# Kernel tuning notes

Measured on AMD Instinct MI355X. Metric: run time of the kernel, lower is better.

Reference implementation:

```python
import jax, jax.numpy as jnp
import numpy as np

N_TX = 1_000_000   # transaction nodes
N_W  = 250_000     # wallet nodes
E    = 2_000_000   # edges per relation
F_TX, F_W = 64, 32 # raw feature dims
H, OUT = 64, 2     # hidden, out (module defaults)


def setup_inputs() -> dict:
    key = jax.random.key(0)
    ks = jax.random.split(key, 40)
    f32 = jnp.float32
    def w(i, shape):
        return jax.random.normal(ks[i], shape, dtype=f32) * 0.05
    inp = {}
    inp["x_tx"] = jax.random.normal(ks[0], (N_TX, F_TX), dtype=f32)
    inp["x_w"]  = jax.random.normal(ks[1], (N_W, F_W), dtype=f32)
    inp["src_tw"] = jax.random.randint(ks[2], (E,), 0, N_TX)
    inp["dst_tw"] = jax.random.randint(ks[3], (E,), 0, N_W)
    inp["src_wt"] = jax.random.randint(ks[4], (E,), 0, N_W)
    inp["dst_wt"] = jax.random.randint(ks[5], (E,), 0, N_TX)
    # lin_in per node type
    inp["Win_tx"], inp["bin_tx"] = w(6, (F_TX, H)), w(7, (H,))
    inp["Win_w"],  inp["bin_w"]  = w(8, (F_W, H)),  w(9, (H,))
    # conv1: SAGEConv per edge type (lin_l has bias, lin_r no bias)
    inp["Wl1_tw"], inp["bl1_tw"], inp["Wr1_tw"] = w(10, (H, H)), w(11, (H,)), w(12, (H, H))
    inp["Wl1_wt"], inp["bl1_wt"], inp["Wr1_wt"] = w(13, (H, H)), w(14, (H,)), w(15, (H, H))
    # conv2
    inp["Wl2_tw"], inp["bl2_tw"], inp["Wr2_tw"] = w(16, (H, H)), w(17, (H,)), w(18, (H, H))
    inp["Wl2_wt"], inp["bl2_wt"], inp["Wr2_wt"] = w(19, (H, H)), w(20, (H,)), w(21, (H, H))
    # tx head
    inp["Wh1"], inp["bh1"] = w(22, (H, H)), w(23, (H,))
    inp["Wh2"], inp["bh2"] = w(24, (H, OUT)), w(25, (OUT,))
    return inp


def _sage(x_src, x_dst, src, dst, Wl, bl, Wr, n_dst):
    # PyG SAGEConv: lin_l(mean_{j->i} x_src[j]) + lin_r(x_dst[i])
    agg = jax.ops.segment_sum(x_src[src], dst, num_segments=n_dst)
    cnt = jax.ops.segment_sum(jnp.ones((src.shape[0],), x_src.dtype), dst,
                              num_segments=n_dst)
    mean = agg / jnp.maximum(cnt, 1.0)[:, None]
    return mean @ Wl + bl + x_dst @ Wr


def reference(x_tx, x_w, src_tw, dst_tw, src_wt, dst_wt,
              Win_tx, bin_tx, Win_w, bin_w,
              Wl1_tw, bl1_tw, Wr1_tw, Wl1_wt, bl1_wt, Wr1_wt,
              Wl2_tw, bl2_tw, Wr2_tw, Wl2_wt, bl2_wt, Wr2_wt,
              Wh1, bh1, Wh2, bh2):
    # per-type input projection
    h_tx = x_tx @ Win_tx + bin_tx   # [N_TX, H]
    h_w  = x_w @ Win_w + bin_w      # [N_W, H]
    # conv1 (HeteroConv aggr='sum'; each dst type has one relation) + relu
    w1 = jax.nn.relu(_sage(h_tx, h_w,  src_tw, dst_tw, Wl1_tw, bl1_tw, Wr1_tw, N_W))
    t1 = jax.nn.relu(_sage(h_w,  h_tx, src_wt, dst_wt, Wl1_wt, bl1_wt, Wr1_wt, N_TX))
    # conv2 + relu
    w2 = jax.nn.relu(_sage(t1, w1, src_tw, dst_tw, Wl2_tw, bl2_tw, Wr2_tw, N_W))
    t2 = jax.nn.relu(_sage(w1, t1, src_wt, dst_wt, Wl2_wt, bl2_wt, Wr2_wt, N_TX))
    # tx head (dropout inactive in eval)
    logits = jax.nn.relu(t2 @ Wh1 + bh1) @ Wh2 + bh2  # [N_TX, 2]
    return (logits, t2, w2)
```

## Files before the change

### kernel.cpp

```cpp
#include <hip/hip_runtime.h>
#include <hip/hip_bf16.h>

typedef __hip_bfloat16 bf16;
typedef __attribute__((ext_vector_type(8))) short bf16x8;
typedef __attribute__((ext_vector_type(4))) float f32x4;

__device__ __forceinline__ float b2f(bf16 v) { return __bfloat162float(v); }
__device__ __forceinline__ bf16 f2b(float v) { return __float2bfloat16(v); }
__device__ __forceinline__ unsigned short f2bb(float v) {
    unsigned int u = __float_as_uint(v);
    u += 0x7fffu + ((u >> 16) & 1u);
    return (unsigned short)(u >> 16);
}
__device__ __forceinline__ float b2fx(bf16x8 v, int k) {
    return __uint_as_float(((unsigned int)(unsigned short)v[k]) << 16);
}

__device__ __forceinline__ f32x4 mfma16(bf16x8 a, bf16x8 b, f32x4 c) {
    return __builtin_amdgcn_mfma_f32_16x16x32_bf16(a, b, c, 0, 0, 0);
}

__device__ __forceinline__ bf16x8 load_bfrag(const float* __restrict__ W, int k0, int col) {
    bf16x8 f;
#pragma unroll
    for (int j = 0; j < 8; ++j)
        f[j] = (short)f2bb(W[(size_t)(k0 + j) * 64 + col]);
    return f;
}

__device__ __forceinline__ int swzH(int row, int b) {
    return row * 128 + (b ^ ((row & 7) << 4));
}

__global__ void count2_kernel(const int* __restrict__ dst_tw, int* __restrict__ deg_w, int ne_tw,
                              const int* __restrict__ dst_wt, int* __restrict__ deg_tx, int ne_wt) {
    int e = blockIdx.x * 256 + threadIdx.x;
    if (e < ne_tw) atomicAdd(&deg_w[dst_tw[e]], 1);
    else {
        int e2 = e - ne_tw;
        if (e2 < ne_wt) atomicAdd(&deg_tx[dst_wt[e2]], 1);
    }
}

__global__ void scan1m_kernel(const int* __restrict__ dw, int* __restrict__ ew,
                              int* __restrict__ pw, int nw, int npw,
                              const int* __restrict__ dt, int* __restrict__ et,
                              int* __restrict__ pt, int nt) {
    __shared__ int sT[256];
    const int* deg; int* excl; int* partial; int n; int b;
    if ((int)blockIdx.x < npw) { deg = dw; excl = ew; partial = pw; n = nw; b = blockIdx.x; }
    else { deg = dt; excl = et; partial = pt; n = nt; b = blockIdx.x - npw; }
    int tid = threadIdx.x;
    int base = b * 1024 + tid * 4;
    int v0 = (base + 0 < n) ? deg[base + 0] : 0;
    int v1 = (base + 1 < n) ? deg[base + 1] : 0;
    int v2 = (base + 2 < n) ? deg[base + 2] : 0;
    int v3 = (base + 3 < n) ? deg[base + 3] : 0;
    int t = v0 + v1 + v2 + v3;
    sT[tid] = t;
    __syncthreads();
    for (int off = 1; off < 256; off <<= 1) {
        int x = (tid >= off) ? sT[tid - off] : 0;
        __syncthreads();
        sT[tid] += x;
        __syncthreads();
    }
    int et2 = sT[tid] - t;
    if (tid == 255) partial[b] = sT[255];
    if (base + 0 < n) excl[base + 0] = et2;
    if (base + 1 < n) excl[base + 1] = et2 + v0;
    if (base + 2 < n) excl[base + 2] = et2 + v0 + v1;
    if (base + 3 < n) excl[base + 3] = et2 + v0 + v1 + v2;
}

__global__ void scan2m_kernel(int* __restrict__ pw, int npw, int* __restrict__ pt, int npt) {
    __shared__ int sT[256];
    __shared__ int carry;
    int* partial = blockIdx.x ? pt : pw;
    int np = blockIdx.x ? npt : npw;
    int tid = threadIdx.x;
    if (tid == 0) carry = 0;
    __syncthreads();
    for (int c = 0; c < np; c += 256) {
        int i = c + tid;
        int v = (i < np) ? partial[i] : 0;
        sT[tid] = v;
        __syncthreads();
        for (int off = 1; off < 256; off <<= 1) {
            int x = (tid >= off) ? sT[tid - off] : 0;
            __syncthreads();
            sT[tid] += x;
            __syncthreads();
        }
        int incl = sT[tid];
        int total = sT[255];
        if (i < np) partial[i] = carry + incl - v;
        __syncthreads();
        if (tid == 0) carry += total;
        __syncthreads();
    }
}

__global__ void scan3m_kernel(const int* __restrict__ ew, const int* __restrict__ pw,
                              int* __restrict__ rw, int* __restrict__ cw, int nw, int nbw,
                              const int* __restrict__ et, const int* __restrict__ pt,
                              int* __restrict__ rt, int* __restrict__ ct, int nt) {
    int b = blockIdx.x;
    const int* excl; const int* partial; int* rp; int* cur; int n; int i;
    if (b < nbw) { i = b * 256 + threadIdx.x; excl = ew; partial = pw; rp = rw; cur = cw; n = nw; }
    else { i = (b - nbw) * 256 + threadIdx.x; excl = et; partial = pt; rp = rt; cur = ct; n = nt; }
    if (i < n) {
        int v = excl[i] + partial[i >> 10];
        rp[i] = v;
        cur[i] = v;
    }
}

__global__ void scatter2_kernel(const int* __restrict__ src_tw, const int* __restrict__ dst_tw,
                                int* __restrict__ cur_w, int* __restrict__ col_tw, int ne_tw,
                                const int* __restrict__ src_wt, const int* __restrict__ dst_wt,
                                int* __restrict__ cur_tx, int* __restrict__ col_wt, int ne_wt) {
    int e = blockIdx.x * 256 + threadIdx.x;
    if (e < ne_tw) {
        int p = atomicAdd(&cur_w[dst_tw[e]], 1);
        col_tw[p] = src_tw[e];
    } else {
        int e2 = e - ne_tw;
        if (e2 < ne_wt) {
            int p = atomicAdd(&cur_tx[dst_wt[e2]], 1);
            col_wt[p] = src_wt[e2];
        }
    }
}

#define GM_ACC(x, w) \
    a0 += (w) * b2fx(x, 0); a1 += (w) * b2fx(x, 1); \
    a2 += (w) * b2fx(x, 2); a3 += (w) * b2fx(x, 3); \
    a4 += (w) * b2fx(x, 4); a5 += (w) * b2fx(x, 5); \
    a6 += (w) * b2fx(x, 6); a7 += (w) * b2fx(x, 7);

__device__ __forceinline__ void gather_body(const bf16* __restrict__ h,
                                            const int* __restrict__ rowptr,
                                            const int* __restrict__ deg,
                                            const int* __restrict__ col,
                                            bf16* __restrict__ mean, int n, int bid) {
    int tid = threadIdx.x;
    int row = bid * 32 + (tid >> 3);
    if (row >= n) return;
    int fg = tid & 7;
    int base = rowptr[row];
    int d = deg[row];
    int lasto = (d > 0) ? d - 1 : 0;
    float a0 = 0.f, a1 = 0.f, a2 = 0.f, a3 = 0.f;
    float a4 = 0.f, a5 = 0.f, a6 = 0.f, a7 = 0.f;
    for (int e0 = 0; e0 < d; e0 += 8) {
        int o1 = (e0 + 1 < d) ? e0 + 1 : lasto;
        int o2 = (e0 + 2 < d) ? e0 + 2 : lasto;
        int o3 = (e0 + 3 < d) ? e0 + 3 : lasto;
        int o4 = (e0 + 4 < d) ? e0 + 4 : lasto;
        int o5 = (e0 + 5 < d) ? e0 + 5 : lasto;
        int o6 = (e0 + 6 < d) ? e0 + 6 : lasto;
        int o7 = (e0 + 7 < d) ? e0 + 7 : lasto;
        int s0 = col[base + e0], s1 = col[base + o1];
        int s2 = col[base + o2], s3 = col[base + o3];
        int s4 = col[base + o4], s5 = col[base + o5];
        int s6 = col[base + o6], s7 = col[base + o7];
        bf16x8 x0 = *(const bf16x8*)(h + ((size_t)s0 << 6) + (fg << 3));
        bf16x8 x1 = *(const bf16x8*)(h + ((size_t)s1 << 6) + (fg << 3));
        bf16x8 x2 = *(const bf16x8*)(h + ((size_t)s2 << 6) + (fg << 3));
        bf16x8 x3 = *(const bf16x8*)(h + ((size_t)s3 << 6) + (fg << 3));
        bf16x8 x4 = *(const bf16x8*)(h + ((size_t)s4 << 6) + (fg << 3));
        bf16x8 x5 = *(const bf16x8*)(h + ((size_t)s5 << 6) + (fg << 3));
        bf16x8 x6 = *(const bf16x8*)(h + ((size_t)s6 << 6) + (fg << 3));
        bf16x8 x7 = *(const bf16x8*)(h + ((size_t)s7 << 6) + (fg << 3));
        float w1 = (e0 + 1 < d) ? 1.f : 0.f;
        float w2 = (e0 + 2 < d) ? 1.f : 0.f;
        float w3 = (e0 + 3 < d) ? 1.f : 0.f;
        float w4 = (e0 + 4 < d) ? 1.f : 0.f;
        float w5 = (e0 + 5 < d) ? 1.f : 0.f;
        float w6 = (e0 + 6 < d) ? 1.f : 0.f;
        float w7 = (e0 + 7 < d) ? 1.f : 0.f;
        GM_ACC(x0, 1.f)
        GM_ACC(x1, w1)
        GM_ACC(x2, w2)
        GM_ACC(x3, w3)
        GM_ACC(x4, w4)
        GM_ACC(x5, w5)
        GM_ACC(x6, w6)
        GM_ACC(x7, w7)
    }
    float dd = fmaxf((float)d, 1.f);
    bf16x8 o;
    o[0] = (short)f2bb(a0 / dd); o[1] = (short)f2bb(a1 / dd);
    o[2] = (short)f2bb(a2 / dd); o[3] = (short)f2bb(a3 / dd);
    o[4] = (short)f2bb(a4 / dd); o[5] = (short)f2bb(a5 / dd);
    o[6] = (short)f2bb(a6 / dd); o[7] = (short)f2bb(a7 / dd);
    *(bf16x8*)(mean + ((size_t)row << 6) + (fg << 3)) = o;
}

__global__ __launch_bounds__(256)
void gather2_kernel(const bf16* __restrict__ hw, const int* __restrict__ rpw,
                    const int* __restrict__ dw, const int* __restrict__ cw,
                    bf16* __restrict__ mw, int nw, int gbw,
                    const bf16* __restrict__ ht, const int* __restrict__ rpt,
                    const int* __restrict__ dt, const int* __restrict__ ct,
                    bf16* __restrict__ mt, int nt) {
    if ((int)blockIdx.x < gbw) gather_body(hw, rpw, dw, cw, mw, nw, blockIdx.x);
    else                       gather_body(ht, rpt, dt, ct, mt, nt, blockIdx.x - gbw);
}

template<bool HEAD>
__device__ __forceinline__ void sage_body(
        const bf16* __restrict__ mean, const bf16* __restrict__ xd,
        const float* __restrict__ Wl, const float* __restrict__ bl,
        const float* __restrict__ Wr,
        float* __restrict__ outf, bf16* __restrict__ outb,
        const float* __restrict__ Wh1, const float* __restrict__ bh1,
        const float* __restrict__ Wh2, const float* __restrict__ bh2,
        float* __restrict__ logits, int n, int bid, short* sH) {
    int tid = threadIdx.x;
    int lane = tid & 63, w = tid >> 6;
    int lm = lane & 15, lq = lane >> 4;

    bf16x8 wc[4][4];
    bf16x8 wh[4][2];
    float blv[4], h1v[4], w2a[4], w2b[4];
#pragma unroll
    for (int ct = 0; ct < 4; ++ct) {
        int colc = ct * 16 + lm;
        wc[ct][0] = load_bfrag(Wl, lq * 8, colc);
        wc[ct][1] = load_bfrag(Wl, 32 + lq * 8, colc);
        wc[ct][2] = load_bfrag(Wr, lq * 8, colc);
        wc[ct][3] = load_bfrag(Wr, 32 + lq * 8, colc);
        blv[ct] = bl[colc];
        if (HEAD) {
            wh[ct][0] = load_bfrag(Wh1, lq * 8, colc);
            wh[ct][1] = load_bfrag(Wh1, 32 + lq * 8, colc);
            h1v[ct] = bh1[colc];
            w2a[ct] = Wh2[colc * 2 + 0];
            w2b[ct] = Wh2[colc * 2 + 1];
        }
    }
    float b20 = 0.f, b21 = 0.f;
    if (HEAD) { b20 = bh2[0]; b21 = bh2[1]; }

    int larow = w * 16 + lm;
    int row0 = bid * 512;
    if (row0 >= n) return;
    int ar = row0 + larow; ar = (ar < n) ? ar : (n - 1);
    const bf16* mrow = mean + ((size_t)ar << 6);
    const bf16* xrow = xd + ((size_t)ar << 6);
    bf16x8 a0 = *(const bf16x8*)(mrow + lq * 8);
    bf16x8 a1 = *(const bf16x8*)(mrow + 32 + lq * 8);
    bf16x8 a2 = *(const bf16x8*)(xrow + lq * 8);
    bf16x8 a3 = *(const bf16x8*)(xrow + 32 + lq * 8);

    for (int g = 0; g < 8; ++g) {
        int gr0 = row0 + g * 64;
        if (gr0 >= n) break;
        bf16x8 n0 = a0, n1 = a1, n2 = a2, n3 = a3;
        if (g < 7) {
            int nr = gr0 + 64 + larow; nr = (nr < n) ? nr : (n - 1);
            const bf16* nm = mean + ((size_t)nr << 6);
            const bf16* nx = xd + ((size_t)nr << 6);
            n0 = *(const bf16x8*)(nm + lq * 8);
            n1 = *(const bf16x8*)(nm + 32 + lq * 8);
            n2 = *(const bf16x8*)(nx + lq * 8);
            n3 = *(const bf16x8*)(nx + 32 + lq * 8);
        }
#pragma unroll
        for (int ct = 0; ct < 4; ++ct) {
            f32x4 acc = {0.f, 0.f, 0.f, 0.f};
            acc = mfma16(a0, wc[ct][0], acc);
            acc = mfma16(a1, wc[ct][1], acc);
            acc = mfma16(a2, wc[ct][2], acc);
            acc = mfma16(a3, wc[ct][3], acc);
            int colc = ct * 16 + lm;
#pragma unroll
            for (int r = 0; r < 4; ++r) {
                int lrow = w * 16 + lq * 4 + r;
                int grow = gr0 + lrow;
                float v = fmaxf(acc[r] + blv[ct], 0.f);
                if (grow < n) {
                    if (outf) outf[(size_t)grow * 64 + colc] = v;
                    if (outb) outb[(size_t)grow * 64 + colc] = f2b(v);
                }
                if (HEAD)
                    *(short*)((char*)sH + swzH(lrow, colc * 2)) = (short)f2bb(v);
            }
        }
        if (HEAD) {
            bf16x8 h0 = *(const bf16x8*)((char*)sH + swzH(larow, lq * 16));
            bf16x8 h1 = *(const bf16x8*)((char*)sH + swzH(larow, 64 + lq * 16));
            float qa0 = 0.f, qa1 = 0.f, qa2 = 0.f, qa3 = 0.f;
            float qb0 = 0.f, qb1 = 0.f, qb2 = 0.f, qb3 = 0.f;
#pragma unroll
            for (int ct = 0; ct < 4; ++ct) {
                f32x4 acc = {0.f, 0.f, 0.f, 0.f};
                acc = mfma16(h0, wh[ct][0], acc);
                acc = mfma16(h1, wh[ct][1], acc);
                float hb = h1v[ct];
                float h_0 = fmaxf(acc[0] + hb, 0.f);
                float h_1 = fmaxf(acc[1] + hb, 0.f);
                float h_2 = fmaxf(acc[2] + hb, 0.f);
                float h_3 = fmaxf(acc[3] + hb, 0.f);
                qa0 += h_0 * w2a[ct]; qb0 += h_0 * w2b[ct];
                qa1 += h_1 * w2a[ct]; qb1 += h_1 * w2b[ct];
                qa2 += h_2 * w2a[ct]; qb2 += h_2 * w2b[ct];
                qa3 += h_3 * w2a[ct]; qb3 += h_3 * w2b[ct];
            }
#pragma unroll
            for (int m = 8; m; m >>= 1) {
                qa0 += __shfl_xor(qa0, m); qb0 += __shfl_xor(qb0, m);
                qa1 += __shfl_xor(qa1, m); qb1 += __shfl_xor(qb1, m);
                qa2 += __shfl_xor(qa2, m); qb2 += __shfl_xor(qb2, m);
                qa3 += __shfl_xor(qa3, m); qb3 += __shfl_xor(qb3, m);
            }
            int rowb = gr0 + w * 16 + lq * 4;
            if (lm == 0) {
                if (rowb + 0 < n) { logits[(size_t)(rowb + 0) * 2 + 0] = qa0 + b20;
                                    logits[(size_t)(rowb + 0) * 2 + 1] = qb0 + b21; }
                if (rowb + 1 < n) { logits[(size_t)(rowb + 1) * 2 + 0] = qa1 + b20;
                                    logits[(size_t)(rowb + 1) * 2 + 1] = qb1 + b21; }
                if (rowb + 2 < n) { logits[(size_t)(rowb + 2) * 2 + 0] = qa2 + b20;
                                    logits[(size_t)(rowb + 2) * 2 + 1] = qb2 + b21; }
                if (rowb + 3 < n) { logits[(size_t)(rowb + 3) * 2 + 0] = qa3 + b20;
                                    logits[(size_t)(rowb + 3) * 2 + 1] = qb3 + b21; }
            }
        }
        a0 = n0; a1 = n1; a2 = n2; a3 = n3;
    }
}

template<bool HEAD>
__global__ __launch_bounds__(256, 2)
void sage2_kernel(const bf16* __restrict__ mw, const bf16* __restrict__ xw,
                  const float* __restrict__ Wlw, const float* __restrict__ blw,
                  const float* __restrict__ Wrw,
                  float* __restrict__ outfw, bf16* __restrict__ outbw, int nw, int gbw,
                  const bf16* __restrict__ mt, const bf16* __restrict__ xt,
                  const float* __restrict__ Wlt, const float* __restrict__ blt,
                  const float* __restrict__ Wrt,
                  float* __restrict__ outft, bf16* __restrict__ outbt,
                  const float* __restrict__ Wh1, const float* __restrict__ bh1,
                  const float* __restrict__ Wh2, const float* __restrict__ bh2,
                  float* __restrict__ logits, int nt) {
    __shared__ __align__(16) short sH[HEAD ? 64 * 64 : 8];
    if ((int)blockIdx.x < gbw)
        sage_body<false>(mw, xw, Wlw, blw, Wrw, outfw, outbw,
                         nullptr, nullptr, nullptr, nullptr, nullptr, nw, blockIdx.x, sH);
    else
        sage_body<HEAD>(mt, xt, Wlt, blt, Wrt, outft, outbt,
                        Wh1, bh1, Wh2, bh2, logits, nt, blockIdx.x - gbw, sH);
}

__global__ __launch_bounds__(256)
void proj64_mfma_kernel(const float* __restrict__ x, const float* __restrict__ W,
                        const float* __restrict__ b, bf16* __restrict__ out, int n) {
    int tid = threadIdx.x;
    int lane = tid & 63, w = tid >> 6;
    int lm = lane & 15, lq = lane >> 4;

    bf16x8 wc[4][2];
    float bv[4];
#pragma unroll
    for (int ct = 0; ct < 4; ++ct) {
        int colc = ct * 16 + lm;
        wc[ct][0] = load_bfrag(W, lq * 8, colc);
        wc[ct][1] = load_bfrag(W, 32 + lq * 8, colc);
        bv[ct] = b[colc];
    }

    int larow = w * 16 + lm;
    int row0 = blockIdx.x * 512;
    if (row0 >= n) return;
    int ar = row0 + larow; ar = (ar < n) ? ar : (n - 1);
    const float* xrow = x + ((size_t)ar << 6);
    float4 p0 = *(const float4*)(xrow + lq * 8);
    float4 p1 = *(const float4*)(xrow + lq * 8 + 4);
    float4 p2 = *(const float4*)(xrow + 32 + lq * 8);
    float4 p3 = *(const float4*)(xrow + 32 + lq * 8 + 4);

    for (int g = 0; g < 8; ++g) {
        int gr0 = row0 + g * 64;
        if (gr0 >= n) break;
        float4 q0 = p0, q1 = p1, q2 = p2, q3 = p3;
        if (g < 7) {
            int nr = gr0 + 64 + larow; nr = (nr < n) ? nr : (n - 1);
            const float* nx = x + ((size_t)nr << 6);
            q0 = *(const float4*)(nx + lq * 8);
            q1 = *(const float4*)(nx + lq * 8 + 4);
            q2 = *(const float4*)(nx + 32 + lq * 8);
            q3 = *(const float4*)(nx + 32 + lq * 8 + 4);
        }
        bf16x8 a0, a1;
        a0[0] = (short)f2bb(p0.x); a0[1] = (short)f2bb(p0.y);
        a0[2] = (short)f2bb(p0.z); a0[3] = (short)f2bb(p0.w);
        a0[4] = (short)f2bb(p1.x); a0[5] = (short)f2bb(p1.y);
        a0[6] = (short)f2bb(p1.z); a0[7] = (short)f2bb(p1.w);
        a1[0] = (short)f2bb(p2.x); a1[1] = (short)f2bb(p2.y);
        a1[2] = (short)f2bb(p2.z); a1[3] = (short)f2bb(p2.w);
        a1[4] = (short)f2bb(p3.x); a1[5] = (short)f2bb(p3.y);
        a1[6] = (short)f2bb(p3.z); a1[7] = (short)f2bb(p3.w);
#pragma unroll
        for (int ct = 0; ct < 4; ++ct) {
            f32x4 acc = {0.f, 0.f, 0.f, 0.f};
            acc = mfma16(a0, wc[ct][0], acc);
            acc = mfma16(a1, wc[ct][1], acc);
            int colc = ct * 16 + lm;
#pragma unroll
            for (int r = 0; r < 4; ++r) {
                int grow = gr0 + w * 16 + lq * 4 + r;
                if (grow < n)
                    out[(size_t)grow * 64 + colc] = f2b(acc[r] + bv[ct]);
            }
        }
        p0 = q0; p1 = q1; p2 = q2; p3 = q3;
    }
}

template<int F>
__global__ void proj_kernel(const float* __restrict__ x, const float* __restrict__ W,
                            const float* __restrict__ b, bf16* __restrict__ out, int n) {
    __shared__ float sW[F][64];
    __shared__ float sb[64];
    __shared__ float sx[16][F];
    int tid = threadIdx.x;
    for (int idx = tid; idx < F * 16; idx += 256)
        ((float4*)sW)[idx] = ((const float4*)W)[idx];
    if (tid < 64) sb[tid] = b[tid];
    int base = blockIdx.x * 64;
    int w = tid >> 6, j = tid & 63;
    int lw = w * 4;
    for (int g = 0; g < 4; ++g) {
        int row0 = base + g * 16;
        __syncthreads();
        for (int idx = tid; idx < 4 * F; idx += 256) {
            int rr = idx / (F / 4), c4 = idx - rr * (F / 4);
            int row = row0 + rr;
            float4 v = (row < n) ? ((const float4*)x)[(size_t)row * (F / 4) + c4]
                                 : make_float4(0.f, 0.f, 0.f, 0.f);
            *(float4*)&sx[rr][c4 * 4] = v;
        }
        __syncthreads();
        float a0 = sb[j], a1 = sb[j], a2 = sb[j], a3 = sb[j];
#pragma unroll 2
        for (int k = 0; k < F; k += 4) {
            float w0 = sW[k][j], w1 = sW[k + 1][j], w2 = sW[k + 2][j], w3 = sW[k + 3][j];
            float4 m0 = *(const float4*)&sx[lw + 0][k];
            float4 m1 = *(const float4*)&sx[lw + 1][k];
            float4 m2 = *(const float4*)&sx[lw + 2][k];
            float4 m3 = *(const float4*)&sx[lw + 3][k];
            a0 += m0.x * w0 + m0.y * w1 + m0.z * w2 + m0.w * w3;
            a1 += m1.x * w0 + m1.y * w1 + m1.z * w2 + m1.w * w3;
            a2 += m2.x * w0 + m2.y * w1 + m2.z * w2 + m2.w * w3;
            a3 += m3.x * w0 + m3.y * w1 + m3.z * w2 + m3.w * w3;
        }
        int r0 = row0 + lw;
        if (r0 + 0 < n) out[(size_t)(r0 + 0) * 64 + j] = f2b(a0);
        if (r0 + 1 < n) out[(size_t)(r0 + 1) * 64 + j] = f2b(a1);
        if (r0 + 2 < n) out[(size_t)(r0 + 2) * 64 + j] = f2b(a2);
        if (r0 + 3 < n) out[(size_t)(r0 + 3) * 64 + j] = f2b(a3);
    }
}

extern "C" void kernel_launch(void* const* d_in, const int* in_sizes, int n_in,
                              void* d_out, int out_size, void* d_ws, size_t ws_size,
                              hipStream_t stream) {
    const float* x_tx   = (const float*)d_in[0];
    const float* x_w    = (const float*)d_in[1];
    const int*   src_tw = (const int*)d_in[2];
    const int*   dst_tw = (const int*)d_in[3];
    const int*   src_wt = (const int*)d_in[4];
    const int*   dst_wt = (const int*)d_in[5];
    const float* Win_tx = (const float*)d_in[6];
    const float* bin_tx = (const float*)d_in[7];
    const float* Win_w  = (const float*)d_in[8];
    const float* bin_w  = (const float*)d_in[9];
    const float* Wl1_tw = (const float*)d_in[10];
    const float* bl1_tw = (const float*)d_in[11];
    const float* Wr1_tw = (const float*)d_in[12];
    const float* Wl1_wt = (const float*)d_in[13];
    const float* bl1_wt = (const float*)d_in[14];
    const float* Wr1_wt = (const float*)d_in[15];
    const float* Wl2_tw = (const float*)d_in[16];
    const float* bl2_tw = (const float*)d_in[17];
    const float* Wr2_tw = (const float*)d_in[18];
    const float* Wl2_wt = (const float*)d_in[19];
    const float* bl2_wt = (const float*)d_in[20];
    const float* Wr2_wt = (const float*)d_in[21];
    const float* Wh1    = (const float*)d_in[22];
    const float* bh1    = (const float*)d_in[23];
    const float* Wh2    = (const float*)d_in[24];
    const float* bh2    = (const float*)d_in[25];

    const int n_tx  = in_sizes[0] / 64;
    const int n_w   = in_sizes[1] / 32;
    const int ne_tw = in_sizes[2];
    const int ne_wt = in_sizes[4];

    bf16* mean_tx = (bf16*)d_ws;
    bf16* mean_w  = mean_tx + (size_t)n_tx * 64;
    bf16* A       = mean_w + (size_t)n_w * 64;
    bf16* B       = A + (size_t)n_tx * 64;
    int*  deg_w   = (int*)(B + (size_t)n_w * 64);
    int*  deg_tx  = deg_w + n_w;
    int*  rp_w    = deg_tx + n_tx;
    int*  rp_tx   = rp_w + n_w;
    int*  cur_w   = rp_tx + n_tx;
    int*  cur_tx  = cur_w + n_w;
    int*  col_tw  = cur_tx + n_tx;
    int*  col_wt  = col_tw + ne_tw;
    int*  part_w  = col_wt + ne_wt;
    int*  part_tx = part_w + 4096;

    float* out_logits = (float*)d_out;
    float* out_t2 = out_logits + (size_t)n_tx * 2;
    float* out_w2 = out_t2 + (size_t)n_tx * 64;

    dim3 blk(256);
    int grid_proj_tx = (n_tx + 511) / 512;
    int grid_proj_w  = (n_w + 63) / 64;
    int gs_w  = (n_w + 511) / 512;
    int gs_tx = (n_tx + 511) / 512;
    int gg_w  = (n_w + 31) / 32;
    int gg_tx = (n_tx + 31) / 32;
    int grid_e = (ne_tw + ne_wt + 255) / 256;
    int np_w  = (n_w + 1023) / 1024;
    int np_tx = (n_tx + 1023) / 1024;
    int nbw = (n_w + 255) / 256;
    int nbt = (n_tx + 255) / 256;

    hipMemsetAsync(deg_w, 0, (size_t)n_w * sizeof(int), stream);
    hipMemsetAsync(deg_tx, 0, (size_t)n_tx * sizeof(int), stream);
    count2_kernel<<<grid_e, blk, 0, stream>>>(dst_tw, deg_w, ne_tw, dst_wt, deg_tx, ne_wt);
    scan1m_kernel<<<np_w + np_tx, blk, 0, stream>>>(deg_w, cur_w, part_w, n_w, np_w,
                                                    deg_tx, cur_tx, part_tx, n_tx);
    scan2m_kernel<<<2, blk, 0, stream>>>(part_w, np_w, part_tx, np_tx);
    scan3m_kernel<<<nbw + nbt, blk, 0, stream>>>(cur_w, part_w, rp_w, cur_w, n_w, nbw,
                                                 cur_tx, part_tx, rp_tx, cur_tx, n_tx);
    scatter2_kernel<<<grid_e, blk, 0, stream>>>(src_tw, dst_tw, cur_w, col_tw, ne_tw,
                                                src_wt, dst_wt, cur_tx, col_wt, ne_wt);

    proj64_mfma_kernel<<<grid_proj_tx, blk, 0, stream>>>(x_tx, Win_tx, bin_tx, A, n_tx);
    proj_kernel<32><<<grid_proj_w, blk, 0, stream>>>(x_w, Win_w, bin_w, B, n_w);

    gather2_kernel<<<gg_w + gg_tx, blk, 0, stream>>>(
        A, rp_w, deg_w, col_tw, mean_w, n_w, gg_w,
        B, rp_tx, deg_tx, col_wt, mean_tx, n_tx);
    sage2_kernel<false><<<gs_w + gs_tx, blk, 0, stream>>>(
        mean_w, B, Wl1_tw, bl1_tw, Wr1_tw, nullptr, B, n_w, gs_w,
        mean_tx, A, Wl1_wt, bl1_wt, Wr1_wt, nullptr, A,
        nullptr, nullptr, nullptr, nullptr, nullptr, n_tx);

    gather2_kernel<<<gg_w + gg_tx, blk, 0, stream>>>(
        A, rp_w, deg_w, col_tw, mean_w, n_w, gg_w,
        B, rp_tx, deg_tx, col_wt, mean_tx, n_tx);
    sage2_kernel<true><<<gs_w + gs_tx, blk, 0, stream>>>(
        mean_w, B, Wl2_tw, bl2_tw, Wr2_tw, out_w2, nullptr, n_w, gs_w,
        mean_tx, A, Wl2_wt, bl2_wt, Wr2_wt, out_t2, nullptr,
        Wh1, bh1, Wh2, bh2, out_logits, n_tx);
}
```

Measured before the change: 1.607 ms.

## Record edge ranks during count and fuse CSR scatter with input projections

The degree-count kernel now stores each edge's atomicAdd return value as its rank within its destination. The scatter step then writes col[rowptr[dst]+rank] with no second round of atomics, and the separate cursor array is dropped. The scatter and both input projection kernels are merged into one launch with block-range dispatch, so projection work can overlap the memory-bound scatter and two launches go away. The cost is extra rank arrays in workspace plus their write and read traffic, and the fused kernel always reserves the projection's shared memory, which can lower occupancy for the scatter blocks.

```diff
diff --git a/kernel.cpp b/kernel.cpp
--- a/kernel.cpp
+++ b/kernel.cpp
@@ -32,13 +32,15 @@
     return row * 128 + (b ^ ((row & 7) << 4));
 }
 
-__global__ void count2_kernel(const int* __restrict__ dst_tw, int* __restrict__ deg_w, int ne_tw,
-                              const int* __restrict__ dst_wt, int* __restrict__ deg_tx, int ne_wt) {
+__global__ void count_rank2_kernel(const int* __restrict__ dst_tw, int* __restrict__ deg_w,
+                                   int* __restrict__ rank_tw, int ne_tw,
+                                   const int* __restrict__ dst_wt, int* __restrict__ deg_tx,
+                                   int* __restrict__ rank_wt, int ne_wt) {
     int e = blockIdx.x * 256 + threadIdx.x;
-    if (e < ne_tw) atomicAdd(&deg_w[dst_tw[e]], 1);
+    if (e < ne_tw) rank_tw[e] = atomicAdd(&deg_w[dst_tw[e]], 1);
     else {
         int e2 = e - ne_tw;
-        if (e2 < ne_wt) atomicAdd(&deg_tx[dst_wt[e2]], 1);
+        if (e2 < ne_wt) rank_wt[e2] = atomicAdd(&deg_tx[dst_wt[e2]], 1);
     }
 }
 
@@ -102,34 +104,155 @@
 }
 
 __global__ void scan3m_kernel(const int* __restrict__ ew, const int* __restrict__ pw,
-                              int* __restrict__ rw, int* __restrict__ cw, int nw, int nbw,
+                              int* __restrict__ rw, int nw, int nbw,
                               const int* __restrict__ et, const int* __restrict__ pt,
-                              int* __restrict__ rt, int* __restrict__ ct, int nt) {
+                              int* __restrict__ rt, int nt) {
     int b = blockIdx.x;
-    const int* excl; const int* partial; int* rp; int* cur; int n; int i;
-    if (b < nbw) { i = b * 256 + threadIdx.x; excl = ew; partial = pw; rp = rw; cur = cw; n = nw; }
-    else { i = (b - nbw) * 256 + threadIdx.x; excl = et; partial = pt; rp = rt; cur = ct; n = nt; }
-    if (i < n) {
-        int v = excl[i] + partial[i >> 10];
-        rp[i] = v;
-        cur[i] = v;
-    }
-}
-
-__global__ void scatter2_kernel(const int* __restrict__ src_tw, const int* __restrict__ dst_tw,
-                                int* __restrict__ cur_w, int* __restrict__ col_tw, int ne_tw,
-                                const int* __restrict__ src_wt, const int* __restrict__ dst_wt,
-                                int* __restrict__ cur_tx, int* __restrict__ col_wt, int ne_wt) {
-    int e = blockIdx.x * 256 + threadIdx.x;
-    if (e < ne_tw) {
-        int p = atomicAdd(&cur_w[dst_tw[e]], 1);
-        col_tw[p] = src_tw[e];
+    const int* excl; const int* partial; int* rp; int n; int i;
+    if (b < nbw) { i = b * 256 + threadIdx.x; excl = ew; partial = pw; rp = rw; n = nw; }
+    else { i = (b - nbw) * 256 + threadIdx.x; excl = et; partial = pt; rp = rt; n = nt; }
+    if (i < n) rp[i] = excl[i] + partial[i >> 10];
+}
+
+__device__ __forceinline__ void proj64_body(const float* __restrict__ x,
+                                            const float* __restrict__ W,
+                                            const float* __restrict__ b,
+                                            bf16* __restrict__ out, int n, int bid) {
+    int tid = threadIdx.x;
+    int lane = tid & 63, w = tid >> 6;
+    int lm = lane & 15, lq = lane >> 4;
+
+    bf16x8 wc[4][2];
+    float bv[4];
+#pragma unroll
+    for (int ct = 0; ct < 4; ++ct) {
+        int colc = ct * 16 + lm;
+        wc[ct][0] = load_bfrag(W, lq * 8, colc);
+        wc[ct][1] = load_bfrag(W, 32 + lq * 8, colc);
+        bv[ct] = b[colc];
+    }
+
+    int larow = w * 16 + lm;
+    int row0 = bid * 512;
+    if (row0 >= n) return;
+    int ar = row0 + larow; ar = (ar < n) ? ar : (n - 1);
+    const float* xrow = x + ((size_t)ar << 6);
+    float4 p0 = *(const float4*)(xrow + lq * 8);
+    float4 p1 = *(const float4*)(xrow + lq * 8 + 4);
+    float4 p2 = *(const float4*)(xrow + 32 + lq * 8);
+    float4 p3 = *(const float4*)(xrow + 32 + lq * 8 + 4);
+
+    for (int g = 0; g < 8; ++g) {
+        int gr0 = row0 + g * 64;
+        if (gr0 >= n) break;
+        float4 q0 = p0, q1 = p1, q2 = p2, q3 = p3;
+        if (g < 7) {
+            int nr = gr0 + 64 + larow; nr = (nr < n) ? nr : (n - 1);
+            const float* nx = x + ((size_t)nr << 6);
+            q0 = *(const float4*)(nx + lq * 8);
+            q1 = *(const float4*)(nx + lq * 8 + 4);
+            q2 = *(const float4*)(nx + 32 + lq * 8);
+            q3 = *(const float4*)(nx + 32 + lq * 8 + 4);
+        }
+        bf16x8 a0, a1;
+        a0[0] = (short)f2bb(p0.x); a0[1] = (short)f2bb(p0.y);
+        a0[2] = (short)f2bb(p0.z); a0[3] = (short)f2bb(p0.w);
+        a0[4] = (short)f2bb(p1.x); a0[5] = (short)f2bb(p1.y);
+        a0[6] = (short)f2bb(p1.z); a0[7] = (short)f2bb(p1.w);
+        a1[0] = (short)f2bb(p2.x); a1[1] = (short)f2bb(p2.y);
+        a1[2] = (short)f2bb(p2.z); a1[3] = (short)f2bb(p2.w);
+        a1[4] = (short)f2bb(p3.x); a1[5] = (short)f2bb(p3.y);
+        a1[6] = (short)f2bb(p3.z); a1[7] = (short)f2bb(p3.w);
+#pragma unroll
+        for (int ct = 0; ct < 4; ++ct) {
+            f32x4 acc = {0.f, 0.f, 0.f, 0.f};
+            acc = mfma16(a0, wc[ct][0], acc);
+            acc = mfma16(a1, wc[ct][1], acc);
+            int colc = ct * 16 + lm;
+#pragma unroll
+            for (int r = 0; r < 4; ++r) {
+                int grow = gr0 + w * 16 + lq * 4 + r;
+                if (grow < n)
+                    out[(size_t)grow * 64 + colc] = f2b(acc[r] + bv[ct]);
+            }
+        }
+        p0 = q0; p1 = q1; p2 = q2; p3 = q3;
+    }
+}
+
+__device__ __forceinline__ void proj32_body(const float* __restrict__ x,
+                                            const float* __restrict__ W,
+                                            const float* __restrict__ b,
+                                            bf16* __restrict__ out, int n, int bid,
+                                            float (*sW)[64], float* sb, float (*sx)[32]) {
+    const int F = 32;
+    int tid = threadIdx.x;
+    for (int idx = tid; idx < F * 16; idx += 256)
+        ((float4*)sW)[idx] = ((const float4*)W)[idx];
+    if (tid < 64) sb[tid] = b[tid];
+    int base = bid * 64;
+    int w = tid >> 6, j = tid & 63;
+    int lw = w * 4;
+    for (int g = 0; g < 4; ++g) {
+        int row0 = base + g * 16;
+        __syncthreads();
+        for (int idx = tid; idx < 4 * F; idx += 256) {
+            int rr = idx / (F / 4), c4 = idx - rr * (F / 4);
+            int row = row0 + rr;
+            float4 v = (row < n) ? ((const float4*)x)[(size_t)row * (F / 4) + c4]
+                                 : make_float4(0.f, 0.f, 0.f, 0.f);
+            *(float4*)&sx[rr][c4 * 4] = v;
+        }
+        __syncthreads();
+        float a0 = sb[j], a1 = sb[j], a2 = sb[j], a3 = sb[j];
+#pragma unroll 2
+        for (int k = 0; k < F; k += 4) {
+            float w0 = sW[k][j], w1 = sW[k + 1][j], w2 = sW[k + 2][j], w3 = sW[k + 3][j];
+            float4 m0 = *(const float4*)&sx[lw + 0][k];
+            float4 m1 = *(const float4*)&sx[lw + 1][k];
+            float4 m2 = *(const float4*)&sx[lw + 2][k];
+            float4 m3 = *(const float4*)&sx[lw + 3][k];
+            a0 += m0.x * w0 + m0.y * w1 + m0.z * w2 + m0.w * w3;
+            a1 += m1.x * w0 + m1.y * w1 + m1.z * w2 + m1.w * w3;
+            a2 += m2.x * w0 + m2.y * w1 + m2.z * w2 + m2.w * w3;
+            a3 += m3.x * w0 + m3.y * w1 + m3.z * w2 + m3.w * w3;
+        }
+        int r0 = row0 + lw;
+        if (r0 + 0 < n) out[(size_t)(r0 + 0) * 64 + j] = f2b(a0);
+        if (r0 + 1 < n) out[(size_t)(r0 + 1) * 64 + j] = f2b(a1);
+        if (r0 + 2 < n) out[(size_t)(r0 + 2) * 64 + j] = f2b(a2);
+        if (r0 + 3 < n) out[(size_t)(r0 + 3) * 64 + j] = f2b(a3);
+    }
+}
+
+__global__ __launch_bounds__(256)
+void fused_front_kernel(const int* __restrict__ src_tw, const int* __restrict__ dst_tw,
+                        const int* __restrict__ rank_tw, const int* __restrict__ rp_w,
+                        int* __restrict__ col_tw, int ne_tw,
+                        const int* __restrict__ src_wt, const int* __restrict__ dst_wt,
+                        const int* __restrict__ rank_wt, const int* __restrict__ rp_tx,
+                        int* __restrict__ col_wt, int ne_wt, int gsc,
+                        const float* __restrict__ x_tx, const float* __restrict__ Win_tx,
+                        const float* __restrict__ bin_tx, bf16* __restrict__ A, int n_tx, int gp64,
+                        const float* __restrict__ x_w, const float* __restrict__ Win_w,
+                        const float* __restrict__ bin_w, bf16* __restrict__ B, int n_w) {
+    __shared__ float sW32[32][64];
+    __shared__ float sb32[64];
+    __shared__ float sx32[16][32];
+    int bid = blockIdx.x;
+    if (bid < gsc) {
+        int e = bid * 256 + threadIdx.x;
+        if (e < ne_tw) {
+            col_tw[rp_w[dst_tw[e]] + rank_tw[e]] = src_tw[e];
+        } else {
+            int e2 = e - ne_tw;
+            if (e2 < ne_wt)
+                col_wt[rp_tx[dst_wt[e2]] + rank_wt[e2]] = src_wt[e2];
+        }
+    } else if (bid < gsc + gp64) {
+        proj64_body(x_tx, Win_tx, bin_tx, A, n_tx, bid - gsc);
     } else {
-        int e2 = e - ne_tw;
-        if (e2 < ne_wt) {
-            int p = atomicAdd(&cur_tx[dst_wt[e2]], 1);
-            col_wt[p] = src_wt[e2];
-        }
+        proj32_body(x_w, Win_w, bin_w, B, n_w, bid - gsc - gp64, sW32, sb32, sx32);
     }
 }
 
@@ -354,116 +477,6 @@
                         Wh1, bh1, Wh2, bh2, logits, nt, blockIdx.x - gbw, sH);
 }
 
-__global__ __launch_bounds__(256)
-void proj64_mfma_kernel(const float* __restrict__ x, const float* __restrict__ W,
-                        const float* __restrict__ b, bf16* __restrict__ out, int n) {
-    int tid = threadIdx.x;
-    int lane = tid & 63, w = tid >> 6;
-    int lm = lane & 15, lq = lane >> 4;
-
-    bf16x8 wc[4][2];
-    float bv[4];
-#pragma unroll
-    for (int ct = 0; ct < 4; ++ct) {
-        int colc = ct * 16 + lm;
-        wc[ct][0] = load_bfrag(W, lq * 8, colc);
-        wc[ct][1] = load_bfrag(W, 32 + lq * 8, colc);
-        bv[ct] = b[colc];
-    }
-
-    int larow = w * 16 + lm;
-    int row0 = blockIdx.x * 512;
-    if (row0 >= n) return;
-    int ar = row0 + larow; ar = (ar < n) ? ar : (n - 1);
-    const float* xrow = x + ((size_t)ar << 6);
-    float4 p0 = *(const float4*)(xrow + lq * 8);
-    float4 p1 = *(const float4*)(xrow + lq * 8 + 4);
-    float4 p2 = *(const float4*)(xrow + 32 + lq * 8);
-    float4 p3 = *(const float4*)(xrow + 32 + lq * 8 + 4);
-
-    for (int g = 0; g < 8; ++g) {
-        int gr0 = row0 + g * 64;
-        if (gr0 >= n) break;
-        float4 q0 = p0, q1 = p1, q2 = p2, q3 = p3;
-        if (g < 7) {
-            int nr = gr0 + 64 + larow; nr = (nr < n) ? nr : (n - 1);
-            const float* nx = x + ((size_t)nr << 6);
-            q0 = *(const float4*)(nx + lq * 8);
-            q1 = *(const float4*)(nx + lq * 8 + 4);
-            q2 = *(const float4*)(nx + 32 + lq * 8);
-            q3 = *(const float4*)(nx + 32 + lq * 8 + 4);
-        }
-        bf16x8 a0, a1;
-        a0[0] = (short)f2bb(p0.x); a0[1] = (short)f2bb(p0.y);
-        a0[2] = (short)f2bb(p0.z); a0[3] = (short)f2bb(p0.w);
-        a0[4] = (short)f2bb(p1.x); a0[5] = (short)f2bb(p1.y);
-        a0[6] = (short)f2bb(p1.z); a0[7] = (short)f2bb(p1.w);
-        a1[0] = (short)f2bb(p2.x); a1[1] = (short)f2bb(p2.y);
-        a1[2] = (short)f2bb(p2.z); a1[3] = (short)f2bb(p2.w);
-        a1[4] = (short)f2bb(p3.x); a1[5] = (short)f2bb(p3.y);
-        a1[6] = (short)f2bb(p3.z); a1[7] = (short)f2bb(p3.w);
-#pragma unroll
-        for (int ct = 0; ct < 4; ++ct) {
-            f32x4 acc = {0.f, 0.f, 0.f, 0.f};
-            acc = mfma16(a0, wc[ct][0], acc);
-            acc = mfma16(a1, wc[ct][1], acc);
-            int colc = ct * 16 + lm;
-#pragma unroll
-            for (int r = 0; r < 4; ++r) {
-                int grow = gr0 + w * 16 + lq * 4 + r;
-                if (grow < n)
-                    out[(size_t)grow * 64 + colc] = f2b(acc[r] + bv[ct]);
-            }
-        }
-        p0 = q0; p1 = q1; p2 = q2; p3 = q3;
-    }
-}
-
-template<int F>
-__global__ void proj_kernel(const float* __restrict__ x, const float* __restrict__ W,
-                            const float* __restrict__ b, bf16* __restrict__ out, int n) {
-    __shared__ float sW[F][64];
-    __shared__ float sb[64];
-    __shared__ float sx[16][F];
-    int tid = threadIdx.x;
-    for (int idx = tid; idx < F * 16; idx += 256)
-        ((float4*)sW)[idx] = ((const float4*)W)[idx];
-    if (tid < 64) sb[tid] = b[tid];
-    int base = blockIdx.x * 64;
-    int w = tid >> 6, j = tid & 63;
-    int lw = w * 4;
-    for (int g = 0; g < 4; ++g) {
-        int row0 = base + g * 16;
-        __syncthreads();
-        for (int idx = tid; idx < 4 * F; idx += 256) {
-            int rr = idx / (F / 4), c4 = idx - rr * (F / 4);
-            int row = row0 + rr;
-            float4 v = (row < n) ? ((const float4*)x)[(size_t)row * (F / 4) + c4]
-                                 : make_float4(0.f, 0.f, 0.f, 0.f);
-            *(float4*)&sx[rr][c4 * 4] = v;
-        }
-        __syncthreads();
-        float a0 = sb[j], a1 = sb[j], a2 = sb[j], a3 = sb[j];
-#pragma unroll 2
-        for (int k = 0; k < F; k += 4) {
-            float w0 = sW[k][j], w1 = sW[k + 1][j], w2 = sW[k + 2][j], w3 = sW[k + 3][j];
-            float4 m0 = *(const float4*)&sx[lw + 0][k];
-            float4 m1 = *(const float4*)&sx[lw + 1][k];
-            float4 m2 = *(const float4*)&sx[lw + 2][k];
-            float4 m3 = *(const float4*)&sx[lw + 3][k];
-            a0 += m0.x * w0 + m0.y * w1 + m0.z * w2 + m0.w * w3;
-            a1 += m1.x * w0 + m1.y * w1 + m1.z * w2 + m1.w * w3;
-            a2 += m2.x * w0 + m2.y * w1 + m2.z * w2 + m2.w * w3;
-            a3 += m3.x * w0 + m3.y * w1 + m3.z * w2 + m3.w * w3;
-        }
-        int r0 = row0 + lw;
-        if (r0 + 0 < n) out[(size_t)(r0 + 0) * 64 + j] = f2b(a0);
-        if (r0 + 1 < n) out[(size_t)(r0 + 1) * 64 + j] = f2b(a1);
-        if (r0 + 2 < n) out[(size_t)(r0 + 2) * 64 + j] = f2b(a2);
-        if (r0 + 3 < n) out[(size_t)(r0 + 3) * 64 + j] = f2b(a3);
-    }
-}
-
 extern "C" void kernel_launch(void* const* d_in, const int* in_sizes, int n_in,
                               void* d_out, int out_size, void* d_ws, size_t ws_size,
                               hipStream_t stream) {
@@ -507,11 +520,13 @@
     int*  deg_tx  = deg_w + n_w;
     int*  rp_w    = deg_tx + n_tx;
     int*  rp_tx   = rp_w + n_w;
-    int*  cur_w   = rp_tx + n_tx;
-    int*  cur_tx  = cur_w + n_w;
-    int*  col_tw  = cur_tx + n_tx;
+    int*  ex_w    = rp_tx + n_tx;
+    int*  ex_tx   = ex_w + n_w;
+    int*  col_tw  = ex_tx + n_tx;
     int*  col_wt  = col_tw + ne_tw;
-    int*  part_w  = col_wt + ne_wt;
+    int*  rank_tw = col_wt + ne_wt;
+    int*  rank_wt = rank_tw + ne_tw;
+    int*  part_w  = rank_wt + ne_wt;
     int*  part_tx = part_w + 4096;
 
     float* out_logits = (float*)d_out;
@@ -519,13 +534,13 @@
     float* out_w2 = out_t2 + (size_t)n_tx * 64;
 
     dim3 blk(256);
-    int grid_proj_tx = (n_tx + 511) / 512;
-    int grid_proj_w  = (n_w + 63) / 64;
+    int gp64 = (n_tx + 511) / 512;
+    int gp32 = (n_w + 63) / 64;
     int gs_w  = (n_w + 511) / 512;
     int gs_tx = (n_tx + 511) / 512;
     int gg_w  = (n_w + 31) / 32;
     int gg_tx = (n_tx + 31) / 32;
-    int grid_e = (ne_tw + ne_wt + 255) / 256;
+    int gsc = (ne_tw + ne_wt + 255) / 256;
     int np_w  = (n_w + 1023) / 1024;
     int np_tx = (n_tx + 1023) / 1024;
     int nbw = (n_w + 255) / 256;
@@ -533,17 +548,19 @@
 
     hipMemsetAsync(deg_w, 0, (size_t)n_w * sizeof(int), stream);
     hipMemsetAsync(deg_tx, 0, (size_t)n_tx * sizeof(int), stream);
-    count2_kernel<<<grid_e, blk, 0, stream>>>(dst_tw, deg_w, ne_tw, dst_wt, deg_tx, ne_wt);
-    scan1m_kernel<<<np_w + np_tx, blk, 0, stream>>>(deg_w, cur_w, part_w, n_w, np_w,
-                                                    deg_tx, cur_tx, part_tx, n_tx);
+    count_rank2_kernel<<<gsc, blk, 0, stream>>>(dst_tw, deg_w, rank_tw, ne_tw,
+                                                dst_wt, deg_tx, rank_wt, ne_wt);
+    scan1m_kernel<<<np_w + np_tx, blk, 0, stream>>>(deg_w, ex_w, part_w, n_w, np_w,
+                                                    deg_tx, ex_tx, part_tx, n_tx);
     scan2m_kernel<<<2, blk, 0, stream>>>(part_w, np_w, part_tx, np_tx);
-    scan3m_kernel<<<nbw + nbt, blk, 0, stream>>>(cur_w, part_w, rp_w, cur_w, n_w, nbw,
-                                                 cur_tx, part_tx, rp_tx, cur_tx, n_tx);
-    scatter2_kernel<<<grid_e, blk, 0, stream>>>(src_tw, dst_tw, cur_w, col_tw, ne_tw,
-                                                src_wt, dst_wt, cur_tx, col_wt, ne_wt);
-
-    proj64_mfma_kernel<<<grid_proj_tx, blk, 0, stream>>>(x_tx, Win_tx, bin_tx, A, n_tx);
-    proj_kernel<32><<<grid_proj_w, blk, 0, stream>>>(x_w, Win_w, bin_w, B, n_w);
+    scan3m_kernel<<<nbw + nbt, blk, 0, stream>>>(ex_w, part_w, rp_w, n_w, nbw,
+                                                 ex_tx, part_tx, rp_tx, n_tx);
+
+    fused_front_kernel<<<gsc + gp64 + gp32, blk, 0, stream>>>(
+        src_tw, dst_tw, rank_tw, rp_w, col_tw, ne_tw,
+        src_wt, dst_wt, rank_wt, rp_tx, col_wt, ne_wt, gsc,
+        x_tx, Win_tx, bin_tx, A, n_tx, gp64,
+        x_w, Win_w, bin_w, B, n_w);
 
     gather2_kernel<<<gg_w + gg_tx, blk, 0, stream>>>(
         A, rp_w, deg_w, col_tw, mean_w, n_w, gg_w,
```

Result: faster. 1.370 ms (-14.8%).
